# Performance work log

Hardware: AMD Instinct MI355X
Metric: run time of the kernel (lower is better)

## Reference

```python
import jax, jax.numpy as jnp
import numpy as np

B, S, D = 4, 2048, 1024
H = 16
HD = D // H  # 64
ROPE_BASE = 10000.0


def _rope_cache(seq_len, dim, dtype=jnp.float32):
    inv_freq = 1.0 / (ROPE_BASE ** (jnp.arange(0, dim, 2, dtype=jnp.float32) / dim))
    t = jnp.arange(seq_len, dtype=jnp.float32)
    freqs = jnp.outer(t, inv_freq)            # [S, dim/2]
    emb = jnp.concatenate([freqs, freqs], -1)  # [S, dim]
    return jnp.cos(emb).astype(dtype), jnp.sin(emb).astype(dtype)


def _rotate_half(x):
    x1, x2 = jnp.split(x, 2, axis=-1)
    return jnp.concatenate([-x2, x1], axis=-1)


def setup_inputs() -> dict:
    key = jax.random.key(0)
    k1, k2, k3 = jax.random.split(key, 3)
    x = jax.random.normal(k1, (B, S, D), dtype=jnp.float32)
    attention_mask = jnp.ones((B, S), dtype=jnp.int32)
    # torch nn.Linear weight is [out, in]; we store [in, out] for x @ W
    w_qkv = jax.random.normal(k2, (D, 3 * D), dtype=jnp.float32) * (1.0 / np.sqrt(D))
    w_out = jax.random.normal(k3, (D, D), dtype=jnp.float32) * (1.0 / np.sqrt(D))
    return {"x": x, "attention_mask": attention_mask, "w_qkv": w_qkv, "w_out": w_out}


def reference(x, attention_mask, w_qkv, w_out):
    b, s, d = x.shape
    qkv = x @ w_qkv                                  # [B,S,3D]
    qkv = qkv.reshape(b, s, 3, H, HD)
    q, k, v = [jnp.transpose(qkv[:, :, i], (0, 2, 1, 3)) for i in range(3)]  # [B,H,S,HD]
    cos, sin = _rope_cache(s, HD, x.dtype)           # [S,HD]
    cos = cos[None, None]                            # [1,1,S,HD]
    sin = sin[None, None]
    q = q * cos + _rotate_half(q) * sin
    k = k * cos + _rotate_half(k) * sin
    scale = 1.0 / np.sqrt(HD)
    scores = jnp.einsum("bhqd,bhkd->bhqk", q, k) * scale  # [B,H,S,S]
    causal = jnp.triu(jnp.ones((s, s), dtype=bool), k=1)
    neg_inf = jnp.finfo(scores.dtype).min
    scores = jnp.where(causal[None, None], -jnp.inf, scores)
    pad = (attention_mask == 0)[:, None, None, :]    # [B,1,1,S]
    scores = jnp.where(pad, -jnp.inf, scores)
    attn = jax.nn.softmax(scores, axis=-1)
    out = jnp.einsum("bhqk,bhkd->bhqd", attn, v)     # [B,H,S,HD]
    out = jnp.transpose(out, (0, 2, 1, 3)).reshape(b, s, d)
    return out @ w_out
```

## Files before the change

kernel.cpp:

```cpp
#include <hip/hip_runtime.h>

#define BQ 4
#define SQ 2048
#define DQ 1024
#define HQ 16
#define BHQ 64

typedef __attribute__((ext_vector_type(8))) short short8;
typedef __attribute__((ext_vector_type(4))) float f32x4;
typedef __attribute__((ext_vector_type(16))) float f32x16;
typedef __attribute__((ext_vector_type(2))) unsigned int u32x2;
typedef unsigned short u16;
typedef unsigned int u32;
typedef unsigned long long u64;

__device__ __forceinline__ u16 f2bf(float f) {
  u32 u = __float_as_uint(f);
  u32 r = u + 0x7fffu + ((u >> 16) & 1u);
  return (u16)(r >> 16);
}
__device__ __forceinline__ float bf2f(u16 h) {
  return __uint_as_float(((u32)h) << 16);
}

__device__ __forceinline__ u32 pkbf(float lo, float hi_) {
  u32 r;
  asm("v_cvt_pk_bf16_f32 %0, %1, %2" : "=v"(r) : "v"(lo), "v"(hi_));
  return r;
}
__device__ __forceinline__ float fexp2(float x) {
  float r;
  asm("v_exp_f32 %0, %1" : "=v"(r) : "v"(x));
  return r;
}
__device__ __forceinline__ float xmax32(float x) { return fmaxf(x, __shfl_xor(x, 32)); }
__device__ __forceinline__ float xsum32(float x) { return x + __shfl_xor(x, 32); }
__device__ __forceinline__ u32 xword(u32 send) { return (u32)__shfl_xor((int)send, 32); }

__device__ __forceinline__ void gload_lds16(const void* g, void* l) {
  __builtin_amdgcn_global_load_lds(
      (const __attribute__((address_space(1))) u32*)(unsigned long long)g,
      (__attribute__((address_space(3))) u32*)(u32)(unsigned long long)l,
      16, 0, 0);
}

__device__ __forceinline__ void transpose_body(const float* __restrict__ in, u16* __restrict__ out,
                                               int R, int C, int bx, int by, int tid) {
  __shared__ float t[32][33];
  int c0 = bx * 32, r0 = by * 32;
  int tx = tid & 31, ty = tid >> 5;
  for (int rr = ty; rr < 32; rr += 8)
    t[rr][tx] = in[(size_t)(r0 + rr) * C + c0 + tx];
  __syncthreads();
  for (int rr = ty; rr < 32; rr += 8)
    out[(size_t)(c0 + rr) * R + r0 + tx] = f2bf(t[tx][rr]);
}

__global__ __launch_bounds__(256) void k_prep(const float* __restrict__ x, u16* __restrict__ xb,
                                              const float* __restrict__ wqkv, u16* __restrict__ wqkvT,
                                              const float* __restrict__ wout, u16* __restrict__ woutT,
                                              float* __restrict__ tab, const int* __restrict__ mask,
                                              u64* __restrict__ mbits) {
  int bid = blockIdx.x, tid = threadIdx.x;
  if (bid < 8192) {
    int i = bid * 256 + tid;
    float4 v = ((const float4*)x)[i];
    ushort4 o;
    o.x = f2bf(v.x); o.y = f2bf(v.y); o.z = f2bf(v.z); o.w = f2bf(v.w);
    ((ushort4*)xb)[i] = o;
  } else if (bid < 11264) {
    int t = bid - 8192;
    transpose_body(wqkv, wqkvT, 1024, 3072, t % 96, t / 96, tid);
  } else if (bid < 12288) {
    int t = bid - 11264;
    transpose_body(wout, woutT, 1024, 1024, t % 32, t / 32, tid);
  } else if (bid < 12544) {
    int i = (bid - 12288) * 256 + tid;
    int s = i >> 5, dp = i & 31;
    float invf = expf(-0.28782313662425576f * (float)dp);
    float ang = (float)s * invf;
    tab[i * 2] = cosf(ang);
    tab[i * 2 + 1] = sinf(ang);
  } else {
    int b = tid >> 6, c = tid & 63;
    int all1 = 1;
    for (int i = 0; i < 32; ++i) all1 &= (mask[b * SQ + c * 32 + i] != 0) ? 1 : 0;
    u64 m = __ballot(all1);
    if (c == 0) mbits[b] = m;
  }
}

template <int EPI>
__global__ __launch_bounds__(256) void k_gemm(const u16* __restrict__ A, const u16* __restrict__ Bt,
                                              float* __restrict__ Cf, u16* __restrict__ qb,
                                              u16* __restrict__ kb, u16* __restrict__ vTs,
                                              const float* __restrict__ tab, int K) {
  __shared__ u16 lA[128 * 64];
  __shared__ u16 lB[128 * 64];
  int bid = blockIdx.x;
  int i_ = bid >> 3;
  int tm = (bid & 7) * 8 + (i_ & 7);
  int tn = i_ >> 3;
  int tid = threadIdx.x, w = tid >> 6, l = tid & 63;
  int wm = w >> 1, wn = w & 1;
  int li = l & 15, lg = l >> 4;
  const u16* gA = A + (size_t)tm * 128 * K;
  const u16* gB = Bt + (size_t)tn * 128 * K;
  f32x4 acc[4][4];
#pragma unroll
  for (int i = 0; i < 4; i++)
#pragma unroll
    for (int j = 0; j < 4; j++) acc[i][j] = (f32x4){0.f, 0.f, 0.f, 0.f};

  int lr = l >> 3, lslot = l & 7;
  int scol = ((lslot ^ lr) * 8);

  for (int kt = 0; kt < K; kt += 64) {
    __syncthreads();
#pragma unroll
    for (int i = 0; i < 4; ++i) {
      int ch = i * 4 + w;
      int row = ch * 8 + lr;
      gload_lds16(gA + (size_t)row * K + kt + scol, &lA[ch * 512]);
      gload_lds16(gB + (size_t)row * K + kt + scol, &lB[ch * 512]);
    }
    __syncthreads();
#pragma unroll
    for (int kk = 0; kk < 2; ++kk) {
      short8 af[4], bfr[4];
#pragma unroll
      for (int mf = 0; mf < 4; ++mf) {
        int row = wm * 64 + mf * 16 + li;
        af[mf] = *(const short8*)&lA[row * 64 + (((kk * 4 + lg)) ^ (row & 7)) * 8];
      }
#pragma unroll
      for (int nf = 0; nf < 4; ++nf) {
        int row = wn * 64 + nf * 16 + li;
        bfr[nf] = *(const short8*)&lB[row * 64 + (((kk * 4 + lg)) ^ (row & 7)) * 8];
      }
#pragma unroll
      for (int mf = 0; mf < 4; ++mf)
#pragma unroll
        for (int nf = 0; nf < 4; ++nf)
          acc[mf][nf] = __builtin_amdgcn_mfma_f32_16x16x32_bf16(af[mf], bfr[nf], acc[mf][nf], 0, 0, 0);
    }
  }
  if (EPI == 0) {
#pragma unroll
    for (int mf = 0; mf < 4; ++mf) {
      int mg0 = tm * 128 + wm * 64 + mf * 16 + lg * 4;
#pragma unroll
      for (int nf = 0; nf < 4; ++nf) {
        int ng = tn * 128 + wn * 64 + nf * 16 + li;
#pragma unroll
        for (int r = 0; r < 4; ++r)
          Cf[(size_t)(mg0 + r) * 1024 + ng] = acc[mf][nf][r];
      }
    }
  } else {
    int which = tn >> 3;
    int h = (tn & 7) * 2 + wn;
    int b = tm >> 4;
    if (which < 2) {
      float scale = (which == 0) ? 0.125f * 1.44269504088896f : 1.0f;
      u16* qk = (which == 0 ? qb : kb) + (((size_t)b * HQ + h) * SQ << 6);
#pragma unroll
      for (int mf = 0; mf < 4; ++mf) {
#pragma unroll
        for (int r = 0; r < 4; ++r) {
          int s = (tm * 128 + wm * 64 + mf * 16 + lg * 4 + r) & 2047;
          u16* dst = qk + ((size_t)s << 6);
#pragma unroll
          for (int nf2 = 0; nf2 < 2; ++nf2) {
            int dp = nf2 * 16 + li;
            float2 cs = *(const float2*)&tab[(s * 32 + dp) * 2];
            float a = acc[mf][nf2][r];
            float bb = acc[mf][nf2 + 2][r];
            dst[dp] = f2bf((a * cs.x - bb * cs.y) * scale);
            dst[dp + 32] = f2bf((bb * cs.x + a * cs.y) * scale);
          }
        }
      }
    } else {
#pragma unroll
      for (int mf = 0; mf < 4; ++mf) {
        int s0 = (tm * 128 + wm * 64 + mf * 16 + lg * 4) & 2047;
        int kt = s0 >> 5, kk0 = s0 & 31;
        int slot = kk0 >> 3;
        size_t tb = (((size_t)(b * HQ + h) * 64 + kt) * 64);
#pragma unroll
        for (int nf = 0; nf < 4; ++nf) {
          int d = nf * 16 + li;
          u32 w0 = pkbf(acc[mf][nf][0], acc[mf][nf][1]);
          u32 w1 = pkbf(acc[mf][nf][2], acc[mf][nf][3]);
          size_t off = (tb + d) * 32 + ((slot ^ ((d >> 1) & 3)) << 3) + (kk0 & 7);
          *(u32x2*)&vTs[off] = (u32x2){w0, w1};
        }
      }
    }
  }
}

__global__ __launch_bounds__(256) void k_flash7(const u16* __restrict__ Q, const u16* __restrict__ Kb,
                                                const u16* __restrict__ VTs, const int* __restrict__ mask,
                                                const u64* __restrict__ mbits, u16* __restrict__ O) {
  __shared__ alignas(16) u16 Kl[2][2048];
  __shared__ alignas(16) u16 Vl[2][2048];
  int bid = blockIdx.x;
  int bh = bid & 63;
  int u = bid >> 6, v = u & 3, k4 = u >> 2;
  int qsup = (k4 == 0) ? v : (k4 == 1) ? 7 - v : (k4 == 2) ? 8 + v : 15 - v;
  int tid = threadIdx.x, w = tid >> 6, l = tid & 63;
  int j = l & 31, hi = l >> 5;
  int myqt = qsup * 4 + w;
  int nt = qsup * 4 + 4;
  int b = bh >> 4, h = bh & 15;
  const int* mp = mask + b * SQ + 4 * hi;
  u64 mb = mbits[b];

  int sr = tid >> 3, sc16 = tid & 7;
  const u16* Kg0 = Kb + ((size_t)bh * SQ) * 64 + sr * 64 + ((sc16 ^ (sr & 7)) * 8);
  const u16* Vg0 = VTs + ((size_t)bh * 64) * 2048 + tid * 8;
  u16* KlB = &Kl[0][(size_t)w * 512];
  u16* VlB = &Vl[0][(size_t)w * 512];

  int qbase = myqt * 32;
  const u16* qp = Q + ((size_t)bh * SQ + qbase + j) * 64 + hi * 8;
  short8 qf[4];
#pragma unroll
  for (int kb = 0; kb < 4; ++kb) qf[kb] = *(const short8*)(qp + kb * 16);

  f32x16 o0, o1;
#pragma unroll
  for (int i = 0; i < 16; ++i) { o0[i] = 0.f; o1[i] = 0.f; }
  float mrun = -INFINITY, lrun = 0.f;

  int swK = (j & 7), swV = (j >> 1) & 3;

  gload_lds16(Kg0, KlB);
  gload_lds16(Vg0, VlB);
  __syncthreads();

  for (int kt = 0; kt < nt; ++kt) {
    int cur = kt & 1;
    if (kt + 1 < nt) {
      gload_lds16(Kg0 + (size_t)(kt + 1) * 2048, KlB + (cur ^ 1) * 2048);
      gload_lds16(Vg0 + (size_t)(kt + 1) * 2048, VlB + (cur ^ 1) * 2048);
    }

    if (kt <= myqt) {
      const u16* Kc = Kl[cur];
      const u16* Vc = Vl[cur];

      short8 kcf[4];
#pragma unroll
      for (int kb = 0; kb < 4; ++kb)
        kcf[kb] = *(const short8*)&Kc[j * 64 + (((hi + 2 * kb)) ^ swK) * 8];

      f32x16 s;
#pragma unroll
      for (int i = 0; i < 16; ++i) s[i] = 0.f;
      __builtin_amdgcn_s_setprio(1);
#pragma unroll
      for (int kb = 0; kb < 4; ++kb)
        s = __builtin_amdgcn_mfma_f32_32x32x16_bf16(kcf[kb], qf[kb], s, 0, 0, 0);
      __builtin_amdgcn_s_setprio(0);

      short8 va0 = *(const short8*)&Vc[j * 32 + ((hi) ^ swV) * 8];
      short8 va1 = *(const short8*)&Vc[j * 32 + ((hi + 2) ^ swV) * 8];
      short8 vb0 = *(const short8*)&Vc[(j + 32) * 32 + ((hi) ^ swV) * 8];
      short8 vb1 = *(const short8*)&Vc[(j + 32) * 32 + ((hi + 2) ^ swV) * 8];

      if (!((mb >> kt) & 1ull)) {
#pragma unroll
        for (int rq = 0; rq < 4; ++rq) {
          int4 mv = *(const int4*)(mp + kt * 32 + 8 * rq);
          if (!mv.x) s[4 * rq + 0] = -INFINITY;
          if (!mv.y) s[4 * rq + 1] = -INFINITY;
          if (!mv.z) s[4 * rq + 2] = -INFINITY;
          if (!mv.w) s[4 * rq + 3] = -INFINITY;
        }
      }
      if (kt == myqt) {
#pragma unroll
        for (int rq = 0; rq < 4; ++rq)
#pragma unroll
          for (int t = 0; t < 4; ++t)
            if (8 * rq + 4 * hi + t > j) s[4 * rq + t] = -INFINITY;
      }

      float t0 = fmaxf(fmaxf(fmaxf(s[0], s[1]), fmaxf(s[2], s[3])),
                       fmaxf(fmaxf(s[4], s[5]), fmaxf(s[6], s[7])));
      t0 = fmaxf(t0, fmaxf(fmaxf(fmaxf(s[8], s[9]), fmaxf(s[10], s[11])),
                           fmaxf(fmaxf(s[12], s[13]), fmaxf(s[14], s[15]))));
      if (!__all(t0 <= mrun + 8.0f)) {
        float tm2 = xmax32(t0);
        float mn = fmaxf(fmaxf(mrun, tm2), -1e30f);
        float alpha = fexp2(mrun - mn);
        mrun = mn;
        lrun *= alpha;
#pragma unroll
        for (int i = 0; i < 16; ++i) { o0[i] *= alpha; o1[i] *= alpha; }
      }
      float ts = 0.f;
#pragma unroll
      for (int i = 0; i < 16; ++i) {
        float pv = fexp2(s[i] - mrun);
        s[i] = pv;
        ts += pv;
      }
      lrun += ts;

      u32 pa[4], pb[4];
#pragma unroll
      for (int q2 = 0; q2 < 4; ++q2) {
        pa[q2] = pkbf(s[4 * q2 + 0], s[4 * q2 + 1]);
        pb[q2] = pkbf(s[4 * q2 + 2], s[4 * q2 + 3]);
      }
      u32 ya01 = xword(hi ? pa[0] : pa[1]);
      u32 yb01 = xword(hi ? pb[0] : pb[1]);
      u32 ya23 = xword(hi ? pa[2] : pa[3]);
      u32 yb23 = xword(hi ? pb[2] : pb[3]);
      union { short8 s8; u32 wd[4]; } f0, f1;
      f0.wd[0] = hi ? ya01 : pa[0];
      f0.wd[1] = hi ? yb01 : pb[0];
      f0.wd[2] = hi ? pa[1] : ya01;
      f0.wd[3] = hi ? pb[1] : yb01;
      f1.wd[0] = hi ? ya23 : pa[2];
      f1.wd[1] = hi ? yb23 : pb[2];
      f1.wd[2] = hi ? pa[3] : ya23;
      f1.wd[3] = hi ? pb[3] : yb23;

      __builtin_amdgcn_s_setprio(1);
      o0 = __builtin_amdgcn_mfma_f32_32x32x16_bf16(va0, f0.s8, o0, 0, 0, 0);
      o0 = __builtin_amdgcn_mfma_f32_32x32x16_bf16(va1, f1.s8, o0, 0, 0, 0);
      o1 = __builtin_amdgcn_mfma_f32_32x32x16_bf16(vb0, f0.s8, o1, 0, 0, 0);
      o1 = __builtin_amdgcn_mfma_f32_32x32x16_bf16(vb1, f1.s8, o1, 0, 0, 0);
      __builtin_amdgcn_s_setprio(0);
    }

    __syncthreads();
  }

  float lfull = xsum32(lrun);
  float inv = 1.0f / lfull;
  u16* ob = O + ((size_t)b * SQ + qbase + j) * DQ + h * 64 + 4 * hi;
#pragma unroll
  for (int q2 = 0; q2 < 4; ++q2) {
#pragma unroll
    for (int e = 0; e < 2; ++e) {
      *(u32*)(ob + 8 * q2 + 2 * e) = pkbf(o0[4 * q2 + 2 * e] * inv, o0[4 * q2 + 2 * e + 1] * inv);
      *(u32*)(ob + 32 + 8 * q2 + 2 * e) = pkbf(o1[4 * q2 + 2 * e] * inv, o1[4 * q2 + 2 * e + 1] * inv);
    }
  }
}

extern "C" void kernel_launch(void* const* d_in, const int* in_sizes, int n_in,
                              void* d_out, int out_size, void* d_ws, size_t ws_size,
                              hipStream_t stream) {
  const float* x = (const float*)d_in[0];
  const int* mask = (const int*)d_in[1];
  const float* wqkv = (const float*)d_in[2];
  const float* wout = (const float*)d_in[3];
  float* out = (float*)d_out;
  char* ws = (char*)d_ws;

  u16* xb    = (u16*)(ws + 0);
  u16* wqkvT = (u16*)(ws + 16777216);
  u16* woutT = (u16*)(ws + 23068672);
  u16* qbuf  = (u16*)(ws + 25165824);
  u16* kbuf  = (u16*)(ws + 41943040);
  u16* vTs   = (u16*)(ws + 75497472);
  u16* attnb = (u16*)(ws + 92274688);
  float* tab = (float*)(ws + 109051904);
  u64* mbits = (u64*)(ws + 109576192);

  k_prep<<<12545, 256, 0, stream>>>(x, xb, wqkv, wqkvT, wout, woutT, tab, mask, mbits);
  k_gemm<1><<<1536, 256, 0, stream>>>(xb, wqkvT, nullptr, qbuf, kbuf, vTs, tab, 1024);
  k_flash7<<<1024, 256, 0, stream>>>(qbuf, kbuf, vTs, mask, mbits, attnb);
  k_gemm<0><<<512, 256, 0, stream>>>(attnb, woutT, out, nullptr, nullptr, nullptr, nullptr, 1024);
}
```

Baseline: 188.0 us.

## Store K and V tiles in MFMA-fragment-major layout instead of XOR swizzle

The QKV projection epilogue now writes K and transposed V into a pre-tiled global layout whose order matches the per-lane fragment order the flash kernel reads. The attention kernel copies each 32-key tile linearly into LDS and reads fragments with contiguous, unswizzled addresses. The goal is to remove the XOR swizzle arithmetic and avoid LDS bank conflicts on fragment loads. In exchange, the epilogue's K stores become scattered 2-byte writes, and the V stores keep their 8-byte writes but lose the swizzle, which may hurt write coalescing in the GEMM.

```diff
diff --git a/kernel.cpp b/kernel.cpp
--- a/kernel.cpp
+++ b/kernel.cpp
@@ -163,21 +163,30 @@
     int b = tm >> 4;
     if (which < 2) {
       float scale = (which == 0) ? 0.125f * 1.44269504088896f : 1.0f;
-      u16* qk = (which == 0 ? qb : kb) + (((size_t)b * HQ + h) * SQ << 6);
+      u16* qk0 = qb + (((size_t)b * HQ + h) * SQ << 6);
+      u16* kb0 = kb + ((size_t)b * HQ + h) * (64 * 2048);
 #pragma unroll
       for (int mf = 0; mf < 4; ++mf) {
 #pragma unroll
         for (int r = 0; r < 4; ++r) {
           int s = (tm * 128 + wm * 64 + mf * 16 + lg * 4 + r) & 2047;
-          u16* dst = qk + ((size_t)s << 6);
 #pragma unroll
           for (int nf2 = 0; nf2 < 2; ++nf2) {
             int dp = nf2 * 16 + li;
             float2 cs = *(const float2*)&tab[(s * 32 + dp) * 2];
             float a = acc[mf][nf2][r];
             float bb = acc[mf][nf2 + 2][r];
-            dst[dp] = f2bf((a * cs.x - bb * cs.y) * scale);
-            dst[dp + 32] = f2bf((bb * cs.x + a * cs.y) * scale);
+            float lo = (a * cs.x - bb * cs.y) * scale;
+            float hi2 = (bb * cs.x + a * cs.y) * scale;
+            if (which == 0) {
+              u16* dst = qk0 + ((size_t)s << 6);
+              dst[dp] = f2bf(lo);
+              dst[dp + 32] = f2bf(hi2);
+            } else {
+              u16* dst = kb0 + (s >> 5) * 2048 + (s & 31) * 8;
+              dst[(dp >> 3) * 256 + (dp & 7)] = f2bf(lo);
+              dst[(dp >> 3) * 256 + 1024 + (dp & 7)] = f2bf(hi2);
+            }
           }
         }
       }
@@ -186,15 +195,13 @@
       for (int mf = 0; mf < 4; ++mf) {
         int s0 = (tm * 128 + wm * 64 + mf * 16 + lg * 4) & 2047;
         int kt = s0 >> 5, kk0 = s0 & 31;
-        int slot = kk0 >> 3;
-        size_t tb = (((size_t)(b * HQ + h) * 64 + kt) * 64);
+        size_t tb = (((size_t)(b * HQ + h) * 64 + kt) * 2048) + (kk0 >> 3) * 512 + (kk0 & 7);
 #pragma unroll
         for (int nf = 0; nf < 4; ++nf) {
           int d = nf * 16 + li;
           u32 w0 = pkbf(acc[mf][nf][0], acc[mf][nf][1]);
           u32 w1 = pkbf(acc[mf][nf][2], acc[mf][nf][3]);
-          size_t off = (tb + d) * 32 + ((slot ^ ((d >> 1) & 3)) << 3) + (kk0 & 7);
-          *(u32x2*)&vTs[off] = (u32x2){w0, w1};
+          *(u32x2*)&vTs[tb + d * 8] = (u32x2){w0, w1};
         }
       }
     }
@@ -218,9 +225,8 @@
   const int* mp = mask + b * SQ + 4 * hi;
   u64 mb = mbits[b];
 
-  int sr = tid >> 3, sc16 = tid & 7;
-  const u16* Kg0 = Kb + ((size_t)bh * SQ) * 64 + sr * 64 + ((sc16 ^ (sr & 7)) * 8);
-  const u16* Vg0 = VTs + ((size_t)bh * 64) * 2048 + tid * 8;
+  const u16* Kg0 = Kb + (size_t)bh * (64 * 2048) + tid * 8;
+  const u16* Vg0 = VTs + (size_t)bh * (64 * 2048) + tid * 8;
   u16* KlB = &Kl[0][(size_t)w * 512];
   u16* VlB = &Vl[0][(size_t)w * 512];
 
@@ -234,8 +240,6 @@
 #pragma unroll
   for (int i = 0; i < 16; ++i) { o0[i] = 0.f; o1[i] = 0.f; }
   float mrun = -INFINITY, lrun = 0.f;
-
-  int swK = (j & 7), swV = (j >> 1) & 3;
 
   gload_lds16(Kg0, KlB);
   gload_lds16(Vg0, VlB);
@@ -255,7 +259,7 @@
       short8 kcf[4];
 #pragma unroll
       for (int kb = 0; kb < 4; ++kb)
-        kcf[kb] = *(const short8*)&Kc[j * 64 + (((hi + 2 * kb)) ^ swK) * 8];
+        kcf[kb] = *(const short8*)&Kc[(hi + 2 * kb) * 256 + j * 8];
 
       f32x16 s;
 #pragma unroll
@@ -266,10 +270,10 @@
         s = __builtin_amdgcn_mfma_f32_32x32x16_bf16(kcf[kb], qf[kb], s, 0, 0, 0);
       __builtin_amdgcn_s_setprio(0);
 
-      short8 va0 = *(const short8*)&Vc[j * 32 + ((hi) ^ swV) * 8];
-      short8 va1 = *(const short8*)&Vc[j * 32 + ((hi + 2) ^ swV) * 8];
-      short8 vb0 = *(const short8*)&Vc[(j + 32) * 32 + ((hi) ^ swV) * 8];
-      short8 vb1 = *(const short8*)&Vc[(j + 32) * 32 + ((hi + 2) ^ swV) * 8];
+      short8 va0 = *(const short8*)&Vc[hi * 512 + j * 8];
+      short8 va1 = *(const short8*)&Vc[(hi + 2) * 512 + j * 8];
+      short8 vb0 = *(const short8*)&Vc[hi * 512 + (j + 32) * 8];
+      short8 vb1 = *(const short8*)&Vc[(hi + 2) * 512 + (j + 32) * 8];
 
       if (!((mb >> kt) & 1ull)) {
 #pragma unroll
```

Result: no change. 185.8 us (-1.2%).
